# Kernel optimization log

Hardware: AMD Instinct MI355X
Metric: run time of the kernel (lower is better)

## Reference

```python
import jax, jax.numpy as jnp
import numpy as np
from jax import lax

T_STEPS = 1024
BATCH = 1024
NUM_STATES = 64


def setup_inputs() -> dict:
    key = jax.random.key(0)
    k_em, k_len, k_start, k_stop, k_trans = jax.random.split(key, 5)
    emission_factors = jax.random.normal(k_em, (T_STEPS, BATCH, NUM_STATES), dtype=jnp.float32)
    sequence_sizes = jax.random.randint(k_len, (BATCH,), 1, T_STEPS + 1, dtype=jnp.int32)
    start_factors = jax.random.normal(k_start, (NUM_STATES,), dtype=jnp.float32)
    stop_factors = jax.random.normal(k_stop, (NUM_STATES,), dtype=jnp.float32)
    transition_factors = jax.random.normal(k_trans, (NUM_STATES, NUM_STATES), dtype=jnp.float32)
    return {
        "emission_factors": emission_factors,
        "sequence_sizes": sequence_sizes,
        "start_factors": start_factors,
        "stop_factors": stop_factors,
        "transition_factors": transition_factors,
    }


def reference(emission_factors, sequence_sizes, start_factors, stop_factors, transition_factors):
    # emission_factors: [T, B, S] time-major; sequence_sizes: [B] lengths in [1, T].
    # Linear-chain CRF forward algorithm (log-partition):
    #   alpha_0   = start + em_0
    #   alpha_t[s] = logsumexp_p(alpha_{t-1}[p] + trans[s, p]) + em_t[s]   (while active)
    #   log_Z     = logsumexp_s(alpha_{L-1}[s] + stop[s])
    # Masked scan: alpha is frozen once a sequence ends, matching the packed
    # variable-batch-size iteration of the original (penultimate_alphas).
    max_steps = emission_factors.shape[0]

    alpha0 = start_factors[None, :] + emission_factors[0]  # [B, S]
    # active[t-1, b] = (t < length_b) for t = 1..T-1
    active = (jnp.arange(1, max_steps)[:, None] < sequence_sizes[None, :])[:, :, None]  # [T-1, B, 1]

    def step(alpha, inp):
        em_t, act = inp  # em_t: [B, S], act: [B, 1]
        # alpha[b, None, p] + trans[None, s, p] -> logsumexp over p
        new_alpha = jax.nn.logsumexp(alpha[:, None, :] + transition_factors[None, :, :], axis=2) + em_t
        return jnp.where(act, new_alpha, alpha), None

    alpha, _ = lax.scan(step, alpha0, (emission_factors[1:], active))
    log_normalizer = jax.nn.logsumexp(alpha + stop_factors[None, :], axis=1)  # [B]
    return log_normalizer
```

## Files before the change

kernel.cpp:

```cpp
#include <hip/hip_runtime.h>

#define T_STEPS 1024
#define BATCH   1024
#define NS      64
#define CPB     16
#define NBLK    (BATCH / CPB)
#define TS      ((size_t)BATCH * NS)

typedef __attribute__((ext_vector_type(8))) __bf16 bf16x8;
typedef __attribute__((ext_vector_type(4))) __bf16 bf16x4;
typedef __attribute__((ext_vector_type(4))) float  f32x4;

#define SWZ_XOR16 0x401F
__device__ __forceinline__ float swz16f(float x) {
    return __uint_as_float((unsigned)__builtin_amdgcn_ds_swizzle(
        (int)__float_as_uint(x), SWZ_XOR16));
}

__global__ __launch_bounds__(64)
void crf_fwd_v9(const float* __restrict__ em,
                const int*   __restrict__ seqlen,
                const float* __restrict__ start,
                const float* __restrict__ stop,
                const float* __restrict__ trans,
                float*       __restrict__ out) {
    __shared__ __align__(16) char Ulds[CPB * 128];

    const int l  = threadIdx.x;
    const int c  = l & 15;
    const int g  = l >> 4;
    const int b0 = blockIdx.x * CPB;
    const int Lc = seqlen[b0 + c];
    const int c7 = c & 7;

    bf16x8 ae[4][2];
#pragma unroll
    for (int mt = 0; mt < 4; ++mt)
#pragma unroll
        for (int ks = 0; ks < 2; ++ks) {
            const float* tp = trans + (size_t)(16 * mt + c) * NS + 32 * ks + 8 * g;
            f32x4 t0 = *(const f32x4*)tp;
            f32x4 t1 = *(const f32x4*)(tp + 4);
            bf16x8 a;
            a[0] = (__bf16)__expf(t0[0]); a[1] = (__bf16)__expf(t0[1]);
            a[2] = (__bf16)__expf(t0[2]); a[3] = (__bf16)__expf(t0[3]);
            a[4] = (__bf16)__expf(t1[0]); a[5] = (__bf16)__expf(t1[1]);
            a[6] = (__bf16)__expf(t1[2]); a[7] = (__bf16)__expf(t1[3]);
            ae[mt][ks] = a;
        }

    float es[4][4], st0[4][4];
#pragma unroll
    for (int mt = 0; mt < 4; ++mt) {
        f32x4 sv = *(const f32x4*)(stop  + 16 * mt + 4 * g);
        f32x4 tv = *(const f32x4*)(start + 16 * mt + 4 * g);
#pragma unroll
        for (int i = 0; i < 4; ++i) { es[mt][i] = __expf(sv[i]); st0[mt][i] = tv[i]; }
    }

    char* ub = (char*)Ulds;
    int woff[4], boff[2];
#pragma unroll
    for (int mt = 0; mt < 4; ++mt)
        woff[mt] = c * 128 + ((((2 * mt + (g >> 1)) ^ c7) << 4) | ((g & 1) << 3));
#pragma unroll
    for (int ks = 0; ks < 2; ++ks)
        boff[ks] = c * 128 + (((4 * ks + g) ^ c7) << 4);

    const float* emp[4];
#pragma unroll
    for (int mt = 0; mt < 4; ++mt)
        emp[mt] = em + (size_t)(b0 + c) * NS + 16 * mt + 4 * g;

    f32x4 emb[4][4];
#pragma unroll
    for (int S = 0; S < 4; ++S)
#pragma unroll
        for (int mt = 0; mt < 4; ++mt)
            emb[S][mt] = *(const f32x4*)(emp[mt] + (size_t)S * TS);

#define CAPTURE_BODY(T_)                                                      \
    do {                                                                      \
        float dv = 0.f;                                                       \
        _Pragma("unroll") for (int m_ = 0; m_ < 4; ++m_)                      \
            _Pragma("unroll") for (int i_ = 0; i_ < 4; ++i_)                  \
                dv = fmaf(u[m_][i_], es[m_][i_], dv);                         \
        dv += swz16f(dv);                                                     \
        dv += __shfl_xor(dv, 32, 64);                                         \
        if ((T_) == Lc - 1 && g == 0) out[b0 + c] = __logf(dv) + c_acc;       \
    } while (0)

#define WRITE_READ()                                                          \
    do {                                                                      \
        bf16x4 p0, p1;                                                        \
        p0[0] = (__bf16)u[0][0]; p0[1] = (__bf16)u[0][1];                     \
        p0[2] = (__bf16)u[0][2]; p0[3] = (__bf16)u[0][3];                     \
        p1[0] = (__bf16)u[1][0]; p1[1] = (__bf16)u[1][1];                     \
        p1[2] = (__bf16)u[1][2]; p1[3] = (__bf16)u[1][3];                     \
        *(bf16x4*)(ub + woff[0]) = p0;                                        \
        *(bf16x4*)(ub + woff[1]) = p1;                                        \
        bfA = *(bf16x8*)(ub + boff[0]);                                       \
        p0[0] = (__bf16)u[2][0]; p0[1] = (__bf16)u[2][1];                     \
        p0[2] = (__bf16)u[2][2]; p0[3] = (__bf16)u[2][3];                     \
        p1[0] = (__bf16)u[3][0]; p1[1] = (__bf16)u[3][1];                     \
        p1[2] = (__bf16)u[3][2]; p1[3] = (__bf16)u[3][3];                     \
        *(bf16x4*)(ub + woff[2]) = p0;                                        \
        *(bf16x4*)(ub + woff[3]) = p1;                                        \
        bfB = *(bf16x8*)(ub + boff[1]);                                       \
    } while (0)

#define STEP(T_, SLOT_, RN_, LAST_)                                           \
    do {                                                                      \
        f32x4 zz = {0.f, 0.f, 0.f, 0.f};                                      \
        f32x4 acc[4];                                                         \
        _Pragma("unroll") for (int m_ = 0; m_ < 4; ++m_)                      \
            acc[m_] = __builtin_amdgcn_mfma_f32_16x16x32_bf16(                \
                ae[m_][0], bfA, zz, 0, 0, 0);                                 \
        _Pragma("unroll") for (int m_ = 0; m_ < 4; ++m_)                      \
            acc[m_] = __builtin_amdgcn_mfma_f32_16x16x32_bf16(                \
                ae[m_][1], bfB, acc[m_], 0, 0, 0);                            \
        if (RN_) {                                                            \
            float v1 = fmaxf(mloc, swz16f(mloc));                             \
            float mm = fmaxf(v1, __shfl_xor(v1, 32, 64));                     \
            mm  = fmaxf(mm, 1e-30f);                                          \
            inv = __builtin_amdgcn_rcpf(mm);                                  \
            c_acc += __logf(mm);                                              \
        }                                                                     \
        _Pragma("unroll") for (int m_ = 0; m_ < 4; ++m_)                      \
            _Pragma("unroll") for (int i_ = 0; i_ < 4; ++i_) {                \
                float exv = __expf(emb[SLOT_][m_][i_]);                       \
                if (RN_) exv *= inv;                                          \
                u[m_][i_] = acc[m_][i_] * exv;                                \
            }                                                                 \
        {        \
            size_t tn = (size_t)(((T_) + 4 <= T_STEPS - 1) ? (T_) + 4         \
                                                           : T_STEPS - 1);    \
            _Pragma("unroll") for (int m_ = 0; m_ < 4; ++m_)                  \
                emb[SLOT_][m_] = *(const f32x4*)(emp[m_] + tn * TS);          \
        }                                                                     \
        if (__any((T_) == Lc - 1)) CAPTURE_BODY(T_);                          \
        if (LAST_) {                                                          \
            mloc = u[0][0];                                                   \
            _Pragma("unroll") for (int m_ = 0; m_ < 4; ++m_)                  \
                _Pragma("unroll") for (int i_ = 0; i_ < 4; ++i_)              \
                    mloc = fmaxf(mloc, u[m_][i_]);                            \
        }                                                                     \
        WRITE_READ();                                                         \
    } while (0)

    float u[4][4];
#pragma unroll
    for (int mt = 0; mt < 4; ++mt)
#pragma unroll
        for (int i = 0; i < 4; ++i)
            u[mt][i] = __expf(st0[mt][i] + emb[0][mt][i]);
#pragma unroll
    for (int mt = 0; mt < 4; ++mt)
        emb[0][mt] = *(const f32x4*)(emp[mt] + 4 * TS);

    float c_acc = 0.f, inv = 1.f;
    (void)inv;
    if (__any(0 == Lc - 1)) CAPTURE_BODY(0);

    float mloc = u[0][0];
#pragma unroll
    for (int mt = 0; mt < 4; ++mt)
#pragma unroll
        for (int i = 0; i < 4; ++i) mloc = fmaxf(mloc, u[mt][i]);

    bf16x8 bfA, bfB;
    WRITE_READ();

    for (int grp = 0; grp < 256; ++grp) {
        const int t0_ = 1 + 4 * grp;
        STEP(t0_ + 0, 1, 1, 0);
        STEP(t0_ + 1, 2, 0, 0);
        STEP(t0_ + 2, 3, 0, 0);
        STEP(t0_ + 3, 0, 0, 1);
    }
}

extern "C" void kernel_launch(void* const* d_in, const int* in_sizes, int n_in,
                              void* d_out, int out_size, void* d_ws, size_t ws_size,
                              hipStream_t stream) {
    const float* em     = (const float*)d_in[0];
    const int*   seqlen = (const int*)  d_in[1];
    const float* start  = (const float*)d_in[2];
    const float* stop   = (const float*)d_in[3];
    const float* trans  = (const float*)d_in[4];
    float*       out    = (float*)d_out;

    crf_fwd_v9<<<NBLK, 64, 0, stream>>>(em, seqlen, start, stop, trans, out);
}
```

Measured before the change: 568.0 us.

## Interleave two independent chain groups per wave to hide MFMA latency

After: 879.1 us. +54.8%, slower.

```diff
diff --git a/kernel.cpp b/kernel.cpp
--- a/kernel.cpp
+++ b/kernel.cpp
@@ -3,8 +3,8 @@
 #define T_STEPS 1024
 #define BATCH   1024
 #define NS      64
-#define CPB     16
-#define NBLK    (BATCH / CPB)
+#define CPW     16
+#define NBLK    (BATCH / (2 * CPW))
 #define TS      ((size_t)BATCH * NS)
 
 typedef __attribute__((ext_vector_type(8))) __bf16 bf16x8;
@@ -18,20 +18,24 @@
 }
 
 __global__ __launch_bounds__(64)
-void crf_fwd_v9(const float* __restrict__ em,
-                const int*   __restrict__ seqlen,
-                const float* __restrict__ start,
-                const float* __restrict__ stop,
-                const float* __restrict__ trans,
-                float*       __restrict__ out) {
-    __shared__ __align__(16) char Ulds[CPB * 128];
+__attribute__((amdgpu_waves_per_eu(1, 1)))
+void crf_fwd_v10(const float* __restrict__ em,
+                 const int*   __restrict__ seqlen,
+                 const float* __restrict__ start,
+                 const float* __restrict__ stop,
+                 const float* __restrict__ trans,
+                 float*       __restrict__ out) {
+    __shared__ __align__(16) char UldsA[CPW * 128];
+    __shared__ __align__(16) char UldsB[CPW * 128];
 
     const int l  = threadIdx.x;
     const int c  = l & 15;
     const int g  = l >> 4;
-    const int b0 = blockIdx.x * CPB;
-    const int Lc = seqlen[b0 + c];
     const int c7 = c & 7;
+    const int obA = blockIdx.x * (2 * CPW) + c;
+    const int obB = obA + CPW;
+    const int LcA = seqlen[obA];
+    const int LcB = seqlen[obB];
 
     bf16x8 ae[4][2];
 #pragma unroll
@@ -49,16 +53,16 @@
             ae[mt][ks] = a;
         }
 
-    float es[4][4], st0[4][4];
+    float es[4][4];
 #pragma unroll
     for (int mt = 0; mt < 4; ++mt) {
-        f32x4 sv = *(const f32x4*)(stop  + 16 * mt + 4 * g);
-        f32x4 tv = *(const f32x4*)(start + 16 * mt + 4 * g);
-#pragma unroll
-        for (int i = 0; i < 4; ++i) { es[mt][i] = __expf(sv[i]); st0[mt][i] = tv[i]; }
+        f32x4 sv = *(const f32x4*)(stop + 16 * mt + 4 * g);
+#pragma unroll
+        for (int i = 0; i < 4; ++i) es[mt][i] = __expf(sv[i]);
     }
 
-    char* ub = (char*)Ulds;
+    char* ubA = (char*)UldsA;
+    char* ubB = (char*)UldsB;
     int woff[4], boff[2];
 #pragma unroll
     for (int mt = 0; mt < 4; ++mt)
@@ -67,116 +71,126 @@
     for (int ks = 0; ks < 2; ++ks)
         boff[ks] = c * 128 + (((4 * ks + g) ^ c7) << 4);
 
-    const float* emp[4];
-#pragma unroll
-    for (int mt = 0; mt < 4; ++mt)
-        emp[mt] = em + (size_t)(b0 + c) * NS + 16 * mt + 4 * g;
-
-    f32x4 emb[4][4];
-#pragma unroll
-    for (int S = 0; S < 4; ++S)
-#pragma unroll
-        for (int mt = 0; mt < 4; ++mt)
-            emb[S][mt] = *(const f32x4*)(emp[mt] + (size_t)S * TS);
-
-#define CAPTURE_BODY(T_)                                                      \
-    do {                                                                      \
-        float dv = 0.f;                                                       \
+    const float* empA = em + (size_t)obA * NS + 4 * g;
+    const float* empB = em + (size_t)obB * NS + 4 * g;
+
+    f32x4 embA[4][4], embB[4][4];
+    float uA[4][4], uB[4][4];
+    f32x4 accA[4], accB[4];
+    bf16x8 bfAA, bfBA, bfAB, bfBB;
+    float mlocA, mlocB, caccA, caccB, invA, invB;
+
+#define CAPT(SF, T_)                                                          \
+    do {                                                                      \
+        float dv_ = 0.f;                                                      \
         _Pragma("unroll") for (int m_ = 0; m_ < 4; ++m_)                      \
             _Pragma("unroll") for (int i_ = 0; i_ < 4; ++i_)                  \
-                dv = fmaf(u[m_][i_], es[m_][i_], dv);                         \
-        dv += swz16f(dv);                                                     \
-        dv += __shfl_xor(dv, 32, 64);                                         \
-        if ((T_) == Lc - 1 && g == 0) out[b0 + c] = __logf(dv) + c_acc;       \
-    } while (0)
-
-#define WRITE_READ()                                                          \
-    do {                                                                      \
-        bf16x4 p0, p1;                                                        \
-        p0[0] = (__bf16)u[0][0]; p0[1] = (__bf16)u[0][1];                     \
-        p0[2] = (__bf16)u[0][2]; p0[3] = (__bf16)u[0][3];                     \
-        p1[0] = (__bf16)u[1][0]; p1[1] = (__bf16)u[1][1];                     \
-        p1[2] = (__bf16)u[1][2]; p1[3] = (__bf16)u[1][3];                     \
-        *(bf16x4*)(ub + woff[0]) = p0;                                        \
-        *(bf16x4*)(ub + woff[1]) = p1;                                        \
-        bfA = *(bf16x8*)(ub + boff[0]);                                       \
-        p0[0] = (__bf16)u[2][0]; p0[1] = (__bf16)u[2][1];                     \
-        p0[2] = (__bf16)u[2][2]; p0[3] = (__bf16)u[2][3];                     \
-        p1[0] = (__bf16)u[3][0]; p1[1] = (__bf16)u[3][1];                     \
-        p1[2] = (__bf16)u[3][2]; p1[3] = (__bf16)u[3][3];                     \
-        *(bf16x4*)(ub + woff[2]) = p0;                                        \
-        *(bf16x4*)(ub + woff[3]) = p1;                                        \
-        bfB = *(bf16x8*)(ub + boff[1]);                                       \
-    } while (0)
-
-#define STEP(T_, SLOT_, RN_, LAST_)                                           \
-    do {                                                                      \
-        f32x4 zz = {0.f, 0.f, 0.f, 0.f};                                      \
-        f32x4 acc[4];                                                         \
-        _Pragma("unroll") for (int m_ = 0; m_ < 4; ++m_)                      \
-            acc[m_] = __builtin_amdgcn_mfma_f32_16x16x32_bf16(                \
-                ae[m_][0], bfA, zz, 0, 0, 0);                                 \
-        _Pragma("unroll") for (int m_ = 0; m_ < 4; ++m_)                      \
-            acc[m_] = __builtin_amdgcn_mfma_f32_16x16x32_bf16(                \
-                ae[m_][1], bfB, acc[m_], 0, 0, 0);                            \
+                dv_ = fmaf(u##SF[m_][i_], es[m_][i_], dv_);                   \
+        dv_ += swz16f(dv_);                                                   \
+        dv_ += __shfl_xor(dv_, 32, 64);                                       \
+        if ((T_) == Lc##SF - 1 && g == 0) out[ob##SF] = __logf(dv_) + cacc##SF; \
+    } while (0)
+
+#define WRR(SF)                                                               \
+    do {                                                                      \
+        bf16x4 q0_, q1_;                                                      \
+        q0_[0] = (__bf16)u##SF[0][0]; q0_[1] = (__bf16)u##SF[0][1];           \
+        q0_[2] = (__bf16)u##SF[0][2]; q0_[3] = (__bf16)u##SF[0][3];           \
+        q1_[0] = (__bf16)u##SF[1][0]; q1_[1] = (__bf16)u##SF[1][1];           \
+        q1_[2] = (__bf16)u##SF[1][2]; q1_[3] = (__bf16)u##SF[1][3];           \
+        *(bf16x4*)(ub##SF + woff[0]) = q0_;                                   \
+        *(bf16x4*)(ub##SF + woff[1]) = q1_;                                   \
+        bfA##SF = *(bf16x8*)(ub##SF + boff[0]);                               \
+        q0_[0] = (__bf16)u##SF[2][0]; q0_[1] = (__bf16)u##SF[2][1];           \
+        q0_[2] = (__bf16)u##SF[2][2]; q0_[3] = (__bf16)u##SF[2][3];           \
+        q1_[0] = (__bf16)u##SF[3][0]; q1_[1] = (__bf16)u##SF[3][1];           \
+        q1_[2] = (__bf16)u##SF[3][2]; q1_[3] = (__bf16)u##SF[3][3];           \
+        *(bf16x4*)(ub##SF + woff[2]) = q0_;                                   \
+        *(bf16x4*)(ub##SF + woff[3]) = q1_;                                   \
+        bfB##SF = *(bf16x8*)(ub##SF + boff[1]);                               \
+    } while (0)
+
+#define MFMAP(SF)                                                             \
+    do {                                                                      \
+        f32x4 zz_ = {0.f, 0.f, 0.f, 0.f};                                     \
+        _Pragma("unroll") for (int m_ = 0; m_ < 4; ++m_)                      \
+            acc##SF[m_] = __builtin_amdgcn_mfma_f32_16x16x32_bf16(            \
+                ae[m_][0], bfA##SF, zz_, 0, 0, 0);                            \
+        _Pragma("unroll") for (int m_ = 0; m_ < 4; ++m_)                      \
+            acc##SF[m_] = __builtin_amdgcn_mfma_f32_16x16x32_bf16(            \
+                ae[m_][1], bfB##SF, acc##SF[m_], 0, 0, 0);                    \
+    } while (0)
+
+#define EPI(SF, T_, SLOT_, RN_, LAST_)                                        \
+    do {                                                                      \
         if (RN_) {                                                            \
-            float v1 = fmaxf(mloc, swz16f(mloc));                             \
-            float mm = fmaxf(v1, __shfl_xor(v1, 32, 64));                     \
-            mm  = fmaxf(mm, 1e-30f);                                          \
-            inv = __builtin_amdgcn_rcpf(mm);                                  \
-            c_acc += __logf(mm);                                              \
+            float v1_ = fmaxf(mloc##SF, swz16f(mloc##SF));                    \
+            float mm_ = fmaxf(v1_, __shfl_xor(v1_, 32, 64));                  \
+            mm_ = fmaxf(mm_, 1e-30f);                                         \
+            inv##SF = __builtin_amdgcn_rcpf(mm_);                             \
+            cacc##SF += __logf(mm_);                                          \
         }                                                                     \
         _Pragma("unroll") for (int m_ = 0; m_ < 4; ++m_)                      \
             _Pragma("unroll") for (int i_ = 0; i_ < 4; ++i_) {                \
-                float exv = __expf(emb[SLOT_][m_][i_]);                       \
-                if (RN_) exv *= inv;                                          \
-                u[m_][i_] = acc[m_][i_] * exv;                                \
+                float exv_ = __expf(emb##SF[SLOT_][m_][i_]);                  \
+                if (RN_) exv_ *= inv##SF;                                     \
+                u##SF[m_][i_] = acc##SF[m_][i_] * exv_;                       \
             }                                                                 \
-        {        \
-            size_t tn = (size_t)(((T_) + 4 <= T_STEPS - 1) ? (T_) + 4         \
-                                                           : T_STEPS - 1);    \
+        {                                                                     \
+            size_t tn_ = (size_t)(((T_) + 4 <= T_STEPS - 1) ? (T_) + 4        \
+                                                            : T_STEPS - 1);   \
+            const float* p_ = emp##SF + tn_ * TS;                             \
             _Pragma("unroll") for (int m_ = 0; m_ < 4; ++m_)                  \
-                emb[SLOT_][m_] = *(const f32x4*)(emp[m_] + tn * TS);          \
-        }                                                                     \
-        if (__any((T_) == Lc - 1)) CAPTURE_BODY(T_);                          \
+                emb##SF[SLOT_][m_] = *(const f32x4*)(p_ + 16 * m_);           \
+        }                                                                     \
+        if (__any((T_) == Lc##SF - 1)) CAPT(SF, T_);                          \
         if (LAST_) {                                                          \
-            mloc = u[0][0];                                                   \
+            mloc##SF = u##SF[0][0];                                           \
             _Pragma("unroll") for (int m_ = 0; m_ < 4; ++m_)                  \
                 _Pragma("unroll") for (int i_ = 0; i_ < 4; ++i_)              \
-                    mloc = fmaxf(mloc, u[m_][i_]);                            \
-        }                                                                     \
-        WRITE_READ();                                                         \
-    } while (0)
-
-    float u[4][4];
-#pragma unroll
-    for (int mt = 0; mt < 4; ++mt)
-#pragma unroll
-        for (int i = 0; i < 4; ++i)
-            u[mt][i] = __expf(st0[mt][i] + emb[0][mt][i]);
-#pragma unroll
-    for (int mt = 0; mt < 4; ++mt)
-        emb[0][mt] = *(const f32x4*)(emp[mt] + 4 * TS);
-
-    float c_acc = 0.f, inv = 1.f;
-    (void)inv;
-    if (__any(0 == Lc - 1)) CAPTURE_BODY(0);
-
-    float mloc = u[0][0];
-#pragma unroll
-    for (int mt = 0; mt < 4; ++mt)
-#pragma unroll
-        for (int i = 0; i < 4; ++i) mloc = fmaxf(mloc, u[mt][i]);
-
-    bf16x8 bfA, bfB;
-    WRITE_READ();
+                    mloc##SF = fmaxf(mloc##SF, u##SF[m_][i_]);                \
+        }                                                                     \
+        WRR(SF);                                                              \
+    } while (0)
+
+#define INIT(SF)                                                              \
+    do {                                                                      \
+        _Pragma("unroll") for (int S_ = 0; S_ < 4; ++S_)                      \
+            _Pragma("unroll") for (int m_ = 0; m_ < 4; ++m_)                  \
+                emb##SF[S_][m_] =                                             \
+                    *(const f32x4*)(emp##SF + (size_t)S_ * TS + 16 * m_);     \
+        _Pragma("unroll") for (int m_ = 0; m_ < 4; ++m_) {                    \
+            f32x4 sv_ = *(const f32x4*)(start + 16 * m_ + 4 * g);             \
+            _Pragma("unroll") for (int i_ = 0; i_ < 4; ++i_)                  \
+                u##SF[m_][i_] = __expf(sv_[i_] + emb##SF[0][m_][i_]);         \
+        }                                                                     \
+        _Pragma("unroll") for (int m_ = 0; m_ < 4; ++m_)                      \
+            emb##SF[0][m_] = *(const f32x4*)(emp##SF + (size_t)4 * TS + 16 * m_); \
+        cacc##SF = 0.f; inv##SF = 1.f; (void)inv##SF;                         \
+        if (__any(0 == Lc##SF - 1)) CAPT(SF, 0);                              \
+        mloc##SF = u##SF[0][0];                                               \
+        _Pragma("unroll") for (int m_ = 0; m_ < 4; ++m_)                      \
+            _Pragma("unroll") for (int i_ = 0; i_ < 4; ++i_)                  \
+                mloc##SF = fmaxf(mloc##SF, u##SF[m_][i_]);                    \
+        WRR(SF);                                                              \
+    } while (0)
+
+#define PAIR(T_, SLOT_, RN_, LAST_)                                           \
+    do {                                                                      \
+        MFMAP(A); MFMAP(B);                                                   \
+        EPI(A, T_, SLOT_, RN_, LAST_);                                        \
+        EPI(B, T_, SLOT_, RN_, LAST_);                                        \
+    } while (0)
+
+    INIT(A);
+    INIT(B);
 
     for (int grp = 0; grp < 256; ++grp) {
         const int t0_ = 1 + 4 * grp;
-        STEP(t0_ + 0, 1, 1, 0);
-        STEP(t0_ + 1, 2, 0, 0);
-        STEP(t0_ + 2, 3, 0, 0);
-        STEP(t0_ + 3, 0, 0, 1);
+        PAIR(t0_ + 0, 1, 1, 0);
+        PAIR(t0_ + 1, 2, 0, 0);
+        PAIR(t0_ + 2, 3, 0, 0);
+        PAIR(t0_ + 3, 0, 0, 1);
     }
 }
 
@@ -190,5 +204,5 @@
     const float* trans  = (const float*)d_in[4];
     float*       out    = (float*)d_out;
 
-    crf_fwd_v9<<<NBLK, 64, 0, stream>>>(em, seqlen, start, stop, trans, out);
+    crf_fwd_v10<<<NBLK, 64, 0, stream>>>(em, seqlen, start, stop, trans, out);
 }
```

## Permute K dimension of transition operand to feed MFMA output directly as B operand

Applied to the files above, without the earlier changes.

Result: faster. 527.4 us (-7.1%).

```diff
diff --git a/kernel.cpp b/kernel.cpp
--- a/kernel.cpp
+++ b/kernel.cpp
@@ -8,7 +8,6 @@
 #define TS      ((size_t)BATCH * NS)
 
 typedef __attribute__((ext_vector_type(8))) __bf16 bf16x8;
-typedef __attribute__((ext_vector_type(4))) __bf16 bf16x4;
 typedef __attribute__((ext_vector_type(4))) float  f32x4;
 
 #define SWZ_XOR16 0x401F
@@ -18,29 +17,26 @@
 }
 
 __global__ __launch_bounds__(64)
-void crf_fwd_v9(const float* __restrict__ em,
-                const int*   __restrict__ seqlen,
-                const float* __restrict__ start,
-                const float* __restrict__ stop,
-                const float* __restrict__ trans,
-                float*       __restrict__ out) {
-    __shared__ __align__(16) char Ulds[CPB * 128];
-
+void crf_fwd_v11(const float* __restrict__ em,
+                 const int*   __restrict__ seqlen,
+                 const float* __restrict__ start,
+                 const float* __restrict__ stop,
+                 const float* __restrict__ trans,
+                 float*       __restrict__ out) {
     const int l  = threadIdx.x;
     const int c  = l & 15;
     const int g  = l >> 4;
     const int b0 = blockIdx.x * CPB;
     const int Lc = seqlen[b0 + c];
-    const int c7 = c & 7;
 
     bf16x8 ae[4][2];
 #pragma unroll
     for (int mt = 0; mt < 4; ++mt)
 #pragma unroll
         for (int ks = 0; ks < 2; ++ks) {
-            const float* tp = trans + (size_t)(16 * mt + c) * NS + 32 * ks + 8 * g;
-            f32x4 t0 = *(const f32x4*)tp;
-            f32x4 t1 = *(const f32x4*)(tp + 4);
+            const float* rp = trans + (size_t)(16 * mt + c) * NS + 32 * ks + 4 * g;
+            f32x4 t0 = *(const f32x4*)rp;
+            f32x4 t1 = *(const f32x4*)(rp + 16);
             bf16x8 a;
             a[0] = (__bf16)__expf(t0[0]); a[1] = (__bf16)__expf(t0[1]);
             a[2] = (__bf16)__expf(t0[2]); a[3] = (__bf16)__expf(t0[3]);
@@ -49,127 +45,112 @@
             ae[mt][ks] = a;
         }
 
-    float es[4][4], st0[4][4];
+    float es[4][4];
 #pragma unroll
     for (int mt = 0; mt < 4; ++mt) {
-        f32x4 sv = *(const f32x4*)(stop  + 16 * mt + 4 * g);
-        f32x4 tv = *(const f32x4*)(start + 16 * mt + 4 * g);
+        f32x4 sv = *(const f32x4*)(stop + 16 * mt + 4 * g);
 #pragma unroll
-        for (int i = 0; i < 4; ++i) { es[mt][i] = __expf(sv[i]); st0[mt][i] = tv[i]; }
+        for (int i = 0; i < 4; ++i) es[mt][i] = __expf(sv[i]);
     }
 
-    char* ub = (char*)Ulds;
-    int woff[4], boff[2];
-#pragma unroll
-    for (int mt = 0; mt < 4; ++mt)
-        woff[mt] = c * 128 + ((((2 * mt + (g >> 1)) ^ c7) << 4) | ((g & 1) << 3));
-#pragma unroll
-    for (int ks = 0; ks < 2; ++ks)
-        boff[ks] = c * 128 + (((4 * ks + g) ^ c7) << 4);
-
-    const float* emp[4];
-#pragma unroll
-    for (int mt = 0; mt < 4; ++mt)
-        emp[mt] = em + (size_t)(b0 + c) * NS + 16 * mt + 4 * g;
+    const float* emp = em + (size_t)(b0 + c) * NS + 4 * g;
 
     f32x4 emb[4][4];
-#pragma unroll
-    for (int S = 0; S < 4; ++S)
-#pragma unroll
-        for (int mt = 0; mt < 4; ++mt)
-            emb[S][mt] = *(const f32x4*)(emp[mt] + (size_t)S * TS);
+    float u[4][4];
+    f32x4 acc[4];
+    bf16x8 bfA, bfB;
+    float mloc, cacc, inv;
 
-#define CAPTURE_BODY(T_)                                                      \
+#define CAPT(T_)                                                              \
     do {                                                                      \
-        float dv = 0.f;                                                       \
+        float dv_ = 0.f;                                                      \
         _Pragma("unroll") for (int m_ = 0; m_ < 4; ++m_)                      \
             _Pragma("unroll") for (int i_ = 0; i_ < 4; ++i_)                  \
-                dv = fmaf(u[m_][i_], es[m_][i_], dv);                         \
-        dv += swz16f(dv);                                                     \
-        dv += __shfl_xor(dv, 32, 64);                                         \
-        if ((T_) == Lc - 1 && g == 0) out[b0 + c] = __logf(dv) + c_acc;       \
+                dv_ = fmaf(u[m_][i_], es[m_][i_], dv_);                       \
+        dv_ += swz16f(dv_);                                                   \
+        dv_ += __shfl_xor(dv_, 32, 64);                                       \
+        if ((T_) == Lc - 1 && g == 0) out[b0 + c] = __logf(dv_) + cacc;       \
     } while (0)
 
-#define WRITE_READ()                                                          \
+#define PACKB()                                                               \
     do {                                                                      \
-        bf16x4 p0, p1;                                                        \
-        p0[0] = (__bf16)u[0][0]; p0[1] = (__bf16)u[0][1];                     \
-        p0[2] = (__bf16)u[0][2]; p0[3] = (__bf16)u[0][3];                     \
-        p1[0] = (__bf16)u[1][0]; p1[1] = (__bf16)u[1][1];                     \
-        p1[2] = (__bf16)u[1][2]; p1[3] = (__bf16)u[1][3];                     \
-        *(bf16x4*)(ub + woff[0]) = p0;                                        \
-        *(bf16x4*)(ub + woff[1]) = p1;                                        \
-        bfA = *(bf16x8*)(ub + boff[0]);                                       \
-        p0[0] = (__bf16)u[2][0]; p0[1] = (__bf16)u[2][1];                     \
-        p0[2] = (__bf16)u[2][2]; p0[3] = (__bf16)u[2][3];                     \
-        p1[0] = (__bf16)u[3][0]; p1[1] = (__bf16)u[3][1];                     \
-        p1[2] = (__bf16)u[3][2]; p1[3] = (__bf16)u[3][3];                     \
-        *(bf16x4*)(ub + woff[2]) = p0;                                        \
-        *(bf16x4*)(ub + woff[3]) = p1;                                        \
-        bfB = *(bf16x8*)(ub + boff[1]);                                       \
+        bf16x8 xa_, xb_;                                                      \
+        xa_[0] = (__bf16)u[0][0]; xa_[1] = (__bf16)u[0][1];                   \
+        xa_[2] = (__bf16)u[0][2]; xa_[3] = (__bf16)u[0][3];                   \
+        xa_[4] = (__bf16)u[1][0]; xa_[5] = (__bf16)u[1][1];                   \
+        xa_[6] = (__bf16)u[1][2]; xa_[7] = (__bf16)u[1][3];                   \
+        xb_[0] = (__bf16)u[2][0]; xb_[1] = (__bf16)u[2][1];                   \
+        xb_[2] = (__bf16)u[2][2]; xb_[3] = (__bf16)u[2][3];                   \
+        xb_[4] = (__bf16)u[3][0]; xb_[5] = (__bf16)u[3][1];                   \
+        xb_[6] = (__bf16)u[3][2]; xb_[7] = (__bf16)u[3][3];                   \
+        bfA = xa_; bfB = xb_;                                                 \
     } while (0)
 
 #define STEP(T_, SLOT_, RN_, LAST_)                                           \
     do {                                                                      \
-        f32x4 zz = {0.f, 0.f, 0.f, 0.f};                                      \
-        f32x4 acc[4];                                                         \
+        f32x4 zz_ = {0.f, 0.f, 0.f, 0.f};                                     \
         _Pragma("unroll") for (int m_ = 0; m_ < 4; ++m_)                      \
             acc[m_] = __builtin_amdgcn_mfma_f32_16x16x32_bf16(                \
-                ae[m_][0], bfA, zz, 0, 0, 0);                                 \
+                ae[m_][0], bfA, zz_, 0, 0, 0);                                \
         _Pragma("unroll") for (int m_ = 0; m_ < 4; ++m_)                      \
             acc[m_] = __builtin_amdgcn_mfma_f32_16x16x32_bf16(                \
                 ae[m_][1], bfB, acc[m_], 0, 0, 0);                            \
         if (RN_) {                                                            \
-            float v1 = fmaxf(mloc, swz16f(mloc));                             \
-            float mm = fmaxf(v1, __shfl_xor(v1, 32, 64));                     \
-            mm  = fmaxf(mm, 1e-30f);                                          \
-            inv = __builtin_amdgcn_rcpf(mm);                                  \
-            c_acc += __logf(mm);                                              \
+            float v1_ = fmaxf(mloc, swz16f(mloc));                            \
+            float mm_ = fmaxf(v1_, __shfl_xor(v1_, 32, 64));                  \
+            mm_ = fmaxf(mm_, 1e-30f);                                         \
+            inv = __builtin_amdgcn_rcpf(mm_);                                 \
+            cacc += __logf(mm_);                                              \
         }                                                                     \
         _Pragma("unroll") for (int m_ = 0; m_ < 4; ++m_)                      \
             _Pragma("unroll") for (int i_ = 0; i_ < 4; ++i_) {                \
-                float exv = __expf(emb[SLOT_][m_][i_]);                       \
-                if (RN_) exv *= inv;                                          \
-                u[m_][i_] = acc[m_][i_] * exv;                                \
+                float exv_ = __expf(emb[SLOT_][m_][i_]);                      \
+                if (RN_) exv_ *= inv;                                         \
+                u[m_][i_] = acc[m_][i_] * exv_;                               \
             }                                                                 \
-        {        \
-            size_t tn = (size_t)(((T_) + 4 <= T_STEPS - 1) ? (T_) + 4         \
-                                                           : T_STEPS - 1);    \
+        {            \
+            size_t tn_ = (size_t)(((T_) + 4 <= T_STEPS - 1) ? (T_) + 4        \
+                                                            : T_STEPS - 1);   \
+            const float* p_ = emp + tn_ * TS;                                 \
             _Pragma("unroll") for (int m_ = 0; m_ < 4; ++m_)                  \
-                emb[SLOT_][m_] = *(const f32x4*)(emp[m_] + tn * TS);          \
+                emb[SLOT_][m_] = *(const f32x4*)(p_ + 16 * m_);               \
         }                                                                     \
-        if (__any((T_) == Lc - 1)) CAPTURE_BODY(T_);                          \
+        if (__any((T_) == Lc - 1)) CAPT(T_);                                  \
         if (LAST_) {                                                          \
             mloc = u[0][0];                                                   \
             _Pragma("unroll") for (int m_ = 0; m_ < 4; ++m_)                  \
                 _Pragma("unroll") for (int i_ = 0; i_ < 4; ++i_)              \
                     mloc = fmaxf(mloc, u[m_][i_]);                            \
         }                                                                     \
-        WRITE_READ();                                                         \
+        PACKB();                                                              \
     } while (0)
 
-    float u[4][4];
+#pragma unroll
+    for (int S = 0; S < 4; ++S)
+#pragma unroll
+        for (int mt = 0; mt < 4; ++mt)
+            emb[S][mt] = *(const f32x4*)(emp + (size_t)S * TS + 16 * mt);
+#pragma unroll
+    for (int mt = 0; mt < 4; ++mt) {
+        f32x4 sv = *(const f32x4*)(start + 16 * mt + 4 * g);
+#pragma unroll
+        for (int i = 0; i < 4; ++i)
+            u[mt][i] = __expf(sv[i] + emb[0][mt][i]);
+    }
 #pragma unroll
     for (int mt = 0; mt < 4; ++mt)
-#pragma unroll
-        for (int i = 0; i < 4; ++i)
-            u[mt][i] = __expf(st0[mt][i] + emb[0][mt][i]);
-#pragma unroll
-    for (int mt = 0; mt < 4; ++mt)
-        emb[0][mt] = *(const f32x4*)(emp[mt] + 4 * TS);
+        emb[0][mt] = *(const f32x4*)(emp + (size_t)4 * TS + 16 * mt);
 
-    float c_acc = 0.f, inv = 1.f;
-    (void)inv;
-    if (__any(0 == Lc - 1)) CAPTURE_BODY(0);
+    cacc = 0.f; inv = 1.f; (void)inv;
+    if (__any(0 == Lc - 1)) CAPT(0);
 
-    float mloc = u[0][0];
+    mloc = u[0][0];
 #pragma unroll
     for (int mt = 0; mt < 4; ++mt)
 #pragma unroll
         for (int i = 0; i < 4; ++i) mloc = fmaxf(mloc, u[mt][i]);
 
-    bf16x8 bfA, bfB;
-    WRITE_READ();
+    PACKB();
 
     for (int grp = 0; grp < 256; ++grp) {
         const int t0_ = 1 + 4 * grp;
@@ -190,5 +171,5 @@
     const float* trans  = (const float*)d_in[4];
     float*       out    = (float*)d_out;
 
-    crf_fwd_v9<<<NBLK, 64, 0, stream>>>(em, seqlen, start, stop, trans, out);
+    crf_fwd_v11<<<NBLK, 64, 0, stream>>>(em, seqlen, start, stop, trans, out);
 }
```
